# Optimization experiments

Hardware: AMD Instinct MI355X
Metric: run time of the kernel (lower is better)

The kernel has to match this reference:

```python
import jax, jax.numpy as jnp
import numpy as np

TEMPERATURE = 8.0  # sqrt(head_dim=64)

def setup_inputs() -> dict:
    key = jax.random.key(0)
    kq, kk, kv, km = jax.random.split(key, 4)
    B, H, S, D = 2, 16, 2048, 64
    q = jax.random.normal(kq, (B, H, S, D), dtype=jnp.float32)
    k = jax.random.normal(kk, (B, H, S, D), dtype=jnp.float32)
    v = jax.random.normal(kv, (B, H, S, D), dtype=jnp.float32)
    mask = jax.random.randint(km, (B, 1, 1, S), 0, 2, dtype=jnp.int32)
    return {"q": q, "k": k, "v": v, "mask": mask}

def reference(q, k, v, mask):
    # attn = softmax((q/T) @ k^T) with mask fill of -1e9 (dropout p=0 -> no-op)
    attn = jnp.einsum("bhsd,bhtd->bhst", q / TEMPERATURE, k)  # [B,H,S,S]
    attn = jnp.where(mask == 0, jnp.float32(-1e9), attn)
    attn = jax.nn.softmax(attn, axis=-1)
    # output = v^T @ attn @ v  -> [B,H,D,D]
    out = jnp.einsum("bhsd,bhst->bhdt", v, attn)   # v.transpose(2,3) @ attn
    out = jnp.einsum("bhdt,bhtc->bhdc", out, v)     # @ v
    return (out, attn)
```

## Files before the change

kernel.cpp:

```cpp
#include <hip/hip_runtime.h>
#include <math.h>

#define S_LEN 2048
#define D_DIM 64
#define NBH   32
#define TINV  0.125f

typedef float  f32x4  __attribute__((ext_vector_type(4)));
typedef short  s16x4  __attribute__((ext_vector_type(4)));
typedef short  s16x8  __attribute__((ext_vector_type(8)));
typedef __bf16 bf16x8 __attribute__((ext_vector_type(8)));

__device__ __forceinline__ short bfc(float f) {
  return __builtin_bit_cast(short, (__bf16)f);
}

__device__ __forceinline__ f32x4 mfma16(s16x8 a, s16x8 b, f32x4 c) {
  return __builtin_amdgcn_mfma_f32_16x16x32_bf16(
      __builtin_bit_cast(bf16x8, a), __builtin_bit_cast(bf16x8, b), c, 0, 0, 0);
}

__global__ __launch_bounds__(256) void prep(
    const float* __restrict__ k, const float* __restrict__ v,
    short* __restrict__ kb16, short* __restrict__ vT)
{
  const int bid = blockIdx.x;
  const int t   = bid & 1023;
  const int bh  = t >> 5;
  const int kt  = t & 31;
  const int tid = threadIdx.x;

  if (bid < 1024) {
    const int st  = tid >> 2;
    const int sd0 = (tid & 3) * 16;
    const float* kp = k + ((size_t)bh * S_LEN + kt * 64 + st) * D_DIM + sd0;
    s16x8 o0, o1;
    #pragma unroll
    for (int j = 0; j < 8; ++j) { o0[j] = bfc(kp[j]); o1[j] = bfc(kp[8 + j]); }
    short* dst = kb16 + ((size_t)bh * S_LEN + kt * 64 + st) * D_DIM + sd0;
    *(s16x8*)dst       = o0;
    *(s16x8*)(dst + 8) = o1;
  } else {
    const int vt0 = (tid & 15) * 4;
    const int vd0 = (tid >> 4) * 4;
    const float* vb = v + ((size_t)bh * S_LEN + kt * 64) * D_DIM;
    f32x4 vr[4];
    #pragma unroll
    for (int i = 0; i < 4; ++i)
      vr[i] = *(const f32x4*)(vb + (size_t)(vt0 + i) * D_DIM + vd0);
    #pragma unroll
    for (int j = 0; j < 4; ++j) {
      s16x4 pk;
      pk[0] = bfc(vr[0][j]); pk[1] = bfc(vr[1][j]);
      pk[2] = bfc(vr[2][j]); pk[3] = bfc(vr[3][j]);
      *(s16x4*)(vT + (size_t)(bh * 64 + vd0 + j) * S_LEN + kt * 64 + vt0) = pk;
    }
  }
}

__global__ __launch_bounds__(256, 4) void attn_fwd(
    const float* __restrict__ q, const short* __restrict__ kb16,
    const short* __restrict__ vT, const int* __restrict__ mask,
    float* __restrict__ attn_out, short* __restrict__ OT)
{
  __shared__ short Kl[64][72];
  __shared__ short Vl[64][72];
  __shared__ short Pl[4][16][72];

  const int bid   = blockIdx.x;
  const int xcd   = bid & 7;
  const int chunk = bid >> 3;
  const int bh    = xcd * 4 + (chunk >> 5);
  const int qt    = chunk & 31;
  const int b     = bh >> 4;

  const int tid  = threadIdx.x;
  const int wave = tid >> 6;
  const int lane = tid & 63;
  const int lr   = lane & 15;
  const int lg   = lane >> 4;
  const int wrow = qt * 64 + wave * 16;

  const short* kbb  = kb16 + (size_t)bh * S_LEN * D_DIM;
  const short* vtb  = vT   + (size_t)bh * 64 * S_LEN;
  const int*   mrow = mask + b * S_LEN;

  s16x8 aq[2];
  {
    const float* qp = q + ((size_t)bh * S_LEN + wrow + lr) * D_DIM + lg * 8;
    #pragma unroll
    for (int kk = 0; kk < 2; ++kk) {
      f32x4 a0 = *(const f32x4*)(qp + kk * 32);
      f32x4 a1 = *(const f32x4*)(qp + kk * 32 + 4);
      s16x8 f;
      #pragma unroll
      for (int j = 0; j < 4; ++j) { f[j] = bfc(a0[j]); f[4 + j] = bfc(a1[j]); }
      aq[kk] = f;
    }
  }

  f32x4 oacc[4];
  #pragma unroll
  for (int n = 0; n < 4; ++n) oacc[n] = (f32x4){0.f, 0.f, 0.f, 0.f};
  float rs = 0.f;

  const int st  = tid >> 2;
  const int sd0 = (tid & 3) * 16;

  s16x8 kr0, kr1, vr0, vr1;
  kr0 = *(const s16x8*)(kbb + (size_t)st * D_DIM + sd0);
  kr1 = *(const s16x8*)(kbb + (size_t)st * D_DIM + sd0 + 8);
  vr0 = *(const s16x8*)(vtb + (size_t)st * S_LEN + sd0);
  vr1 = *(const s16x8*)(vtb + (size_t)st * S_LEN + sd0 + 8);

  for (int kt = 0; kt < 32; ++kt) {
    __syncthreads();
    *(s16x8*)&Kl[st][sd0]     = kr0;
    *(s16x8*)&Kl[st][sd0 + 8] = kr1;
    *(s16x8*)&Vl[st][sd0]     = vr0;
    *(s16x8*)&Vl[st][sd0 + 8] = vr1;

    if (kt + 1 < 32) {
      kr0 = *(const s16x8*)(kbb + (size_t)((kt + 1) * 64 + st) * D_DIM + sd0);
      kr1 = *(const s16x8*)(kbb + (size_t)((kt + 1) * 64 + st) * D_DIM + sd0 + 8);
      vr0 = *(const s16x8*)(vtb + (size_t)st * S_LEN + (kt + 1) * 64 + sd0);
      vr1 = *(const s16x8*)(vtb + (size_t)st * S_LEN + (kt + 1) * 64 + sd0 + 8);
    }

    const unsigned long long mbits = __ballot(mrow[kt * 64 + lane] != 0);
    __syncthreads();

    #pragma unroll
    for (int n = 0; n < 4; ++n) {
      f32x4 sacc = (f32x4){0.f, 0.f, 0.f, 0.f};
      #pragma unroll
      for (int kk = 0; kk < 2; ++kk) {
        s16x8 bk = *(const s16x8*)&Kl[n * 16 + lr][kk * 32 + lg * 8];
        sacc = mfma16(bk, aq[kk], sacc);
      }
      const unsigned nib = (unsigned)(mbits >> (n * 16 + lg * 4)) & 0xFu;
      s16x4 pk;
      #pragma unroll
      for (int reg = 0; reg < 4; ++reg) {
        float e = __expf(sacc[reg] * TINV);
        float p = (nib & (1u << reg)) ? e : 0.f;
        rs += p;
        pk[reg] = bfc(p);
      }
      *(s16x4*)&Pl[wave][lr][n * 16 + lg * 4] = pk;
    }

    #pragma unroll
    for (int kk = 0; kk < 2; ++kk) {
      s16x8 ap = *(const s16x8*)&Pl[wave][lr][kk * 32 + lg * 8];
      #pragma unroll
      for (int n = 0; n < 4; ++n) {
        s16x8 bv = *(const s16x8*)&Vl[n * 16 + lr][kk * 32 + lg * 8];
        oacc[n] = mfma16(ap, bv, oacc[n]);
      }
    }
  }

  rs += __shfl_xor(rs, 16, 64);
  rs += __shfl_xor(rs, 32, 64);
  const float rinv = 1.0f / rs;

  float rinvO[4];
  #pragma unroll
  for (int reg = 0; reg < 4; ++reg)
    rinvO[reg] = __shfl(rinv, lg * 4 + reg, 64);

  #pragma unroll
  for (int n = 0; n < 4; ++n) {
    s16x4 ov;
    #pragma unroll
    for (int reg = 0; reg < 4; ++reg) ov[reg] = bfc(oacc[n][reg] * rinvO[reg]);
    short* dst = OT + (size_t)(bh * 64 + n * 16 + lr) * S_LEN + wrow + lg * 4;
    *(s16x4*)dst = ov;
  }

  float* ap_out = attn_out + (size_t)bh * S_LEN * S_LEN + (size_t)(wrow + lr) * S_LEN;

  for (int kt = 0; kt < 32; ++kt) {
    const unsigned long long mbits = __ballot(mrow[kt * 64 + lane] != 0);

    #pragma unroll
    for (int n = 0; n < 4; ++n) {
      f32x4 sacc = (f32x4){0.f, 0.f, 0.f, 0.f};
      #pragma unroll
      for (int kk = 0; kk < 2; ++kk) {
        s16x8 bk = *(const s16x8*)(kbb + (size_t)(kt * 64 + n * 16 + lr) * D_DIM +
                                   kk * 32 + lg * 8);
        sacc = mfma16(bk, aq[kk], sacc);
      }
      const unsigned nib = (unsigned)(mbits >> (n * 16 + lg * 4)) & 0xFu;
      f32x4 pv;
      #pragma unroll
      for (int reg = 0; reg < 4; ++reg) {
        float e = __expf(sacc[reg] * TINV);
        pv[reg] = (nib & (1u << reg)) ? e * rinv : 0.f;
      }
      __builtin_nontemporal_store(pv, (f32x4*)(ap_out + kt * 64 + n * 16 + lg * 4));
    }
  }
}

__global__ __launch_bounds__(256) void vo_gemm(
    const short* __restrict__ vT, const short* __restrict__ OT,
    float* __restrict__ out)
{
  const int bh   = blockIdx.x;
  const int tid  = threadIdx.x;
  const int wave = tid >> 6;
  const int lane = tid & 63;
  const int lr   = lane & 15;
  const int lg   = lane >> 4;

  const short* vb = vT + (size_t)(bh * 64) * S_LEN;
  const short* ob = OT + (size_t)(bh * 64) * S_LEN;

  f32x4 acc[4];
  #pragma unroll
  for (int n = 0; n < 4; ++n) acc[n] = (f32x4){0.f, 0.f, 0.f, 0.f};

  for (int s = 0; s < S_LEN; s += 32) {
    s16x8 a = *(const s16x8*)&vb[(size_t)(wave * 16 + lr) * S_LEN + s + lg * 8];
    #pragma unroll
    for (int n = 0; n < 4; ++n) {
      s16x8 bo = *(const s16x8*)&ob[(size_t)(n * 16 + lr) * S_LEN + s + lg * 8];
      acc[n] = mfma16(a, bo, acc[n]);
    }
  }

  #pragma unroll
  for (int n = 0; n < 4; ++n) {
    #pragma unroll
    for (int reg = 0; reg < 4; ++reg) {
      const int d = wave * 16 + lg * 4 + reg;
      const int c = n * 16 + lr;
      out[(size_t)(bh * 64 + d) * 64 + c] = acc[n][reg];
    }
  }
}

extern "C" void kernel_launch(void* const* d_in, const int* in_sizes, int n_in,
                              void* d_out, int out_size, void* d_ws, size_t ws_size,
                              hipStream_t stream) {
  (void)in_sizes; (void)n_in; (void)out_size; (void)ws_size;
  const float* q    = (const float*)d_in[0];
  const float* k    = (const float*)d_in[1];
  const float* v    = (const float*)d_in[2];
  const int*   mask = (const int*)d_in[3];

  float* out  = (float*)d_out;
  float* attn = out + (size_t)NBH * 64 * 64;

  short* OT   = (short*)d_ws;
  short* vT   = (short*)d_ws + (size_t)NBH * 64 * S_LEN;
  short* kb16 = (short*)d_ws + (size_t)NBH * 64 * S_LEN * 2;

  prep<<<dim3(2048), dim3(256), 0, stream>>>(k, v, kb16, vT);
  attn_fwd<<<dim3(1024), dim3(256), 0, stream>>>(q, kb16, vT, mask, attn, OT);
  vo_gemm<<<dim3(NBH), dim3(256), 0, stream>>>(vT, OT, out);
}
```

Baseline: 244.8 us.

## Use 32x32 MFMA with register P exchange and swizzled LDS in first pass

Rewrites the first attention pass to use 32x32x16 bf16 MFMAs. Waves are split into two query tiles by two key halves. The P tile is passed from the score MFMA to the PV MFMA through v_permlane32_swap instead of a per-wave LDS staging buffer, and K/V are stored in XOR-swizzled unpadded LDS to avoid bank conflicts. Partial row sums and output accumulators from the two key halves are reduced through LDS at the end. The aim is to raise MFMA efficiency and cut LDS traffic, at the cost of more registers, an extra cross-wave reduction and inline asm that only works on recent CDNA parts.

```diff
diff --git a/kernel.cpp b/kernel.cpp
--- a/kernel.cpp
+++ b/kernel.cpp
@@ -6,18 +6,31 @@
 #define NBH   32
 #define TINV  0.125f
 
-typedef float  f32x4  __attribute__((ext_vector_type(4)));
-typedef short  s16x4  __attribute__((ext_vector_type(4)));
-typedef short  s16x8  __attribute__((ext_vector_type(8)));
-typedef __bf16 bf16x8 __attribute__((ext_vector_type(8)));
+typedef float  f32x4   __attribute__((ext_vector_type(4)));
+typedef float  f32x16  __attribute__((ext_vector_type(16)));
+typedef short  s16x4   __attribute__((ext_vector_type(4)));
+typedef short  s16x8   __attribute__((ext_vector_type(8)));
+typedef unsigned u32x4 __attribute__((ext_vector_type(4)));
+typedef __bf16 bf16x8  __attribute__((ext_vector_type(8)));
 
 __device__ __forceinline__ short bfc(float f) {
   return __builtin_bit_cast(short, (__bf16)f);
+}
+__device__ __forceinline__ unsigned pk2(float lo, float hi) {
+  return (unsigned)(unsigned short)bfc(lo) | ((unsigned)(unsigned short)bfc(hi) << 16);
 }
 
 __device__ __forceinline__ f32x4 mfma16(s16x8 a, s16x8 b, f32x4 c) {
   return __builtin_amdgcn_mfma_f32_16x16x32_bf16(
       __builtin_bit_cast(bf16x8, a), __builtin_bit_cast(bf16x8, b), c, 0, 0, 0);
+}
+__device__ __forceinline__ f32x16 mfma32(s16x8 a, s16x8 b, f32x16 c) {
+  return __builtin_amdgcn_mfma_f32_32x32x16_bf16(
+      __builtin_bit_cast(bf16x8, a), __builtin_bit_cast(bf16x8, b), c, 0, 0, 0);
+}
+
+__device__ __forceinline__ short* ldsp(short* base, int row, int byteoff) {
+  return (short*)((char*)base + row * 128 + (byteoff ^ ((row & 7) << 4)));
 }
 
 __global__ __launch_bounds__(256) void prep(
@@ -63,9 +76,11 @@
     const short* __restrict__ vT, const int* __restrict__ mask,
     float* __restrict__ attn_out, short* __restrict__ OT)
 {
-  __shared__ short Kl[64][72];
-  __shared__ short Vl[64][72];
-  __shared__ short Pl[4][16][72];
+  __shared__ short KV[2][64][64];
+  __shared__ float rspart[4][32];
+
+  short* KlB = &KV[0][0][0];
+  short* VlB = &KV[1][0][0];
 
   const int bid   = blockIdx.x;
   const int xcd   = bid & 7;
@@ -79,107 +94,146 @@
   const int lane = tid & 63;
   const int lr   = lane & 15;
   const int lg   = lane >> 4;
-  const int wrow = qt * 64 + wave * 16;
+  const int L31  = lane & 31;
+  const int hi   = lane >> 5;
+  const int Q0   = qt * 64;
+
+  const int qtile = wave & 1;
+  const int tt    = wave >> 1;
 
   const short* kbb  = kb16 + (size_t)bh * S_LEN * D_DIM;
   const short* vtb  = vT   + (size_t)bh * 64 * S_LEN;
   const int*   mrow = mask + b * S_LEN;
 
+  s16x8 aqv[4];
+  {
+    const float* qp = q + ((size_t)bh * S_LEN + Q0 + qtile * 32 + L31) * D_DIM + hi * 8;
+    #pragma unroll
+    for (int ks = 0; ks < 4; ++ks) {
+      f32x4 x0 = *(const f32x4*)(qp + ks * 16);
+      f32x4 x1 = *(const f32x4*)(qp + ks * 16 + 4);
+      s16x8 f;
+      #pragma unroll
+      for (int j = 0; j < 4; ++j) { f[j] = bfc(x0[j]); f[4 + j] = bfc(x1[j]); }
+      aqv[ks] = f;
+    }
+  }
+
+  f32x16 oacc[2];
+  #pragma unroll
+  for (int dt = 0; dt < 2; ++dt)
+    #pragma unroll
+    for (int r = 0; r < 16; ++r) oacc[dt][r] = 0.f;
+  float rs = 0.f;
+
+  const int st = tid >> 2;
+  const int c0 = (tid & 3) * 32;
+
+  s16x8 kr0, kr1, vr0, vr1;
+  kr0 = *(const s16x8*)(kbb + (size_t)st * D_DIM + c0 / 2);
+  kr1 = *(const s16x8*)(kbb + (size_t)st * D_DIM + c0 / 2 + 8);
+  vr0 = *(const s16x8*)(vtb + (size_t)st * S_LEN + c0 / 2);
+  vr1 = *(const s16x8*)(vtb + (size_t)st * S_LEN + c0 / 2 + 8);
+
+  for (int kt = 0; kt < 32; ++kt) {
+    __syncthreads();
+    *(s16x8*)ldsp(KlB, st, c0)      = kr0;
+    *(s16x8*)ldsp(KlB, st, c0 + 16) = kr1;
+    *(s16x8*)ldsp(VlB, st, c0)      = vr0;
+    *(s16x8*)ldsp(VlB, st, c0 + 16) = vr1;
+    __syncthreads();
+
+    if (kt + 1 < 32) {
+      kr0 = *(const s16x8*)(kbb + (size_t)((kt + 1) * 64 + st) * D_DIM + c0 / 2);
+      kr1 = *(const s16x8*)(kbb + (size_t)((kt + 1) * 64 + st) * D_DIM + c0 / 2 + 8);
+      vr0 = *(const s16x8*)(vtb + (size_t)st * S_LEN + (kt + 1) * 64 + c0 / 2);
+      vr1 = *(const s16x8*)(vtb + (size_t)st * S_LEN + (kt + 1) * 64 + c0 / 2 + 8);
+    }
+    const unsigned long long mbits = __ballot(mrow[kt * 64 + lane] != 0);
+
+    f32x16 sacc;
+    #pragma unroll
+    for (int r = 0; r < 16; ++r) sacc[r] = 0.f;
+    #pragma unroll
+    for (int ks = 0; ks < 4; ++ks) {
+      s16x8 ak = *(const s16x8*)ldsp(KlB, tt * 32 + L31, ks * 32 + hi * 16);
+      sacc = mfma32(ak, aqv[ks], sacc);
+    }
+
+    const unsigned mloc = (unsigned)(mbits >> (tt * 32 + hi * 4));
+    #pragma unroll
+    for (int r = 0; r < 16; ++r) {
+      float e = __expf(sacc[r] * TINV);
+      e = ((mloc >> ((r & 3) + 8 * (r >> 2))) & 1u) ? e : 0.f;
+      rs += e;
+      sacc[r] = e;
+    }
+
+    unsigned a0 = pk2(sacc[0], sacc[1]),   b0 = pk2(sacc[4], sacc[5]);
+    unsigned a1 = pk2(sacc[2], sacc[3]),   b1 = pk2(sacc[6], sacc[7]);
+    unsigned a2 = pk2(sacc[8], sacc[9]),   b2 = pk2(sacc[12], sacc[13]);
+    unsigned a3 = pk2(sacc[10], sacc[11]), b3 = pk2(sacc[14], sacc[15]);
+    asm volatile("v_permlane32_swap_b32 %0, %1" : "+v"(a0), "+v"(b0));
+    asm volatile("v_permlane32_swap_b32 %0, %1" : "+v"(a1), "+v"(b1));
+    asm volatile("v_permlane32_swap_b32 %0, %1" : "+v"(a2), "+v"(b2));
+    asm volatile("v_permlane32_swap_b32 %0, %1" : "+v"(a3), "+v"(b3));
+    const s16x8 pb0 = __builtin_bit_cast(s16x8, (u32x4){a0, a1, b0, b1});
+    const s16x8 pb1 = __builtin_bit_cast(s16x8, (u32x4){a2, a3, b2, b3});
+
+    #pragma unroll
+    for (int dt = 0; dt < 2; ++dt) {
+      s16x8 bv0 = *(const s16x8*)ldsp(VlB, dt * 32 + L31, tt * 64 + hi * 16);
+      s16x8 bv1 = *(const s16x8*)ldsp(VlB, dt * 32 + L31, tt * 64 + 32 + hi * 16);
+      oacc[dt] = mfma32(bv0, pb0, oacc[dt]);
+      oacc[dt] = mfma32(bv1, pb1, oacc[dt]);
+    }
+  }
+
+  rs += __shfl_xor(rs, 32, 64);
+
+  __syncthreads();
+  if (lane < 32) rspart[wave][lane] = rs;
+  float* oex = (float*)&KV[0][0][0];
+  if (wave >= 2) {
+    #pragma unroll
+    for (int dt = 0; dt < 2; ++dt)
+      #pragma unroll
+      for (int r = 0; r < 16; ++r)
+        oex[(wave - 2) * 2048 + dt * 1024 + r * 64 + lane] = oacc[dt][r];
+  }
+  __syncthreads();
+
+  if (wave < 2) {
+    const float rinvq = 1.0f / (rspart[wave][L31] + rspart[wave + 2][L31]);
+    #pragma unroll
+    for (int dt = 0; dt < 2; ++dt)
+      #pragma unroll
+      for (int r = 0; r < 16; ++r) {
+        const int d = dt * 32 + (r & 3) + 8 * (r >> 2) + 4 * hi;
+        float val = (oacc[dt][r] + oex[wave * 2048 + dt * 1024 + r * 64 + lane]) * rinvq;
+        OT[(size_t)(bh * 64 + d) * S_LEN + Q0 + wave * 32 + L31] = bfc(val);
+      }
+  }
+
+  const int qin = (wave & 1) * 16 + lr;
+  const float rinv = 1.0f / (rspart[wave >> 1][qin] + rspart[(wave >> 1) + 2][qin]);
+
   s16x8 aq[2];
   {
-    const float* qp = q + ((size_t)bh * S_LEN + wrow + lr) * D_DIM + lg * 8;
+    const float* qp = q + ((size_t)bh * S_LEN + Q0 + wave * 16 + lr) * D_DIM + lg * 8;
     #pragma unroll
     for (int kk = 0; kk < 2; ++kk) {
-      f32x4 a0 = *(const f32x4*)(qp + kk * 32);
-      f32x4 a1 = *(const f32x4*)(qp + kk * 32 + 4);
+      f32x4 x0 = *(const f32x4*)(qp + kk * 32);
+      f32x4 x1 = *(const f32x4*)(qp + kk * 32 + 4);
       s16x8 f;
       #pragma unroll
-      for (int j = 0; j < 4; ++j) { f[j] = bfc(a0[j]); f[4 + j] = bfc(a1[j]); }
+      for (int j = 0; j < 4; ++j) { f[j] = bfc(x0[j]); f[4 + j] = bfc(x1[j]); }
       aq[kk] = f;
     }
   }
 
-  f32x4 oacc[4];
-  #pragma unroll
-  for (int n = 0; n < 4; ++n) oacc[n] = (f32x4){0.f, 0.f, 0.f, 0.f};
-  float rs = 0.f;
-
-  const int st  = tid >> 2;
-  const int sd0 = (tid & 3) * 16;
-
-  s16x8 kr0, kr1, vr0, vr1;
-  kr0 = *(const s16x8*)(kbb + (size_t)st * D_DIM + sd0);
-  kr1 = *(const s16x8*)(kbb + (size_t)st * D_DIM + sd0 + 8);
-  vr0 = *(const s16x8*)(vtb + (size_t)st * S_LEN + sd0);
-  vr1 = *(const s16x8*)(vtb + (size_t)st * S_LEN + sd0 + 8);
-
-  for (int kt = 0; kt < 32; ++kt) {
-    __syncthreads();
-    *(s16x8*)&Kl[st][sd0]     = kr0;
-    *(s16x8*)&Kl[st][sd0 + 8] = kr1;
-    *(s16x8*)&Vl[st][sd0]     = vr0;
-    *(s16x8*)&Vl[st][sd0 + 8] = vr1;
-
-    if (kt + 1 < 32) {
-      kr0 = *(const s16x8*)(kbb + (size_t)((kt + 1) * 64 + st) * D_DIM + sd0);
-      kr1 = *(const s16x8*)(kbb + (size_t)((kt + 1) * 64 + st) * D_DIM + sd0 + 8);
-      vr0 = *(const s16x8*)(vtb + (size_t)st * S_LEN + (kt + 1) * 64 + sd0);
-      vr1 = *(const s16x8*)(vtb + (size_t)st * S_LEN + (kt + 1) * 64 + sd0 + 8);
-    }
-
-    const unsigned long long mbits = __ballot(mrow[kt * 64 + lane] != 0);
-    __syncthreads();
-
-    #pragma unroll
-    for (int n = 0; n < 4; ++n) {
-      f32x4 sacc = (f32x4){0.f, 0.f, 0.f, 0.f};
-      #pragma unroll
-      for (int kk = 0; kk < 2; ++kk) {
-        s16x8 bk = *(const s16x8*)&Kl[n * 16 + lr][kk * 32 + lg * 8];
-        sacc = mfma16(bk, aq[kk], sacc);
-      }
-      const unsigned nib = (unsigned)(mbits >> (n * 16 + lg * 4)) & 0xFu;
-      s16x4 pk;
-      #pragma unroll
-      for (int reg = 0; reg < 4; ++reg) {
-        float e = __expf(sacc[reg] * TINV);
-        float p = (nib & (1u << reg)) ? e : 0.f;
-        rs += p;
-        pk[reg] = bfc(p);
-      }
-      *(s16x4*)&Pl[wave][lr][n * 16 + lg * 4] = pk;
-    }
-
-    #pragma unroll
-    for (int kk = 0; kk < 2; ++kk) {
-      s16x8 ap = *(const s16x8*)&Pl[wave][lr][kk * 32 + lg * 8];
-      #pragma unroll
-      for (int n = 0; n < 4; ++n) {
-        s16x8 bv = *(const s16x8*)&Vl[n * 16 + lr][kk * 32 + lg * 8];
-        oacc[n] = mfma16(ap, bv, oacc[n]);
-      }
-    }
-  }
-
-  rs += __shfl_xor(rs, 16, 64);
-  rs += __shfl_xor(rs, 32, 64);
-  const float rinv = 1.0f / rs;
-
-  float rinvO[4];
-  #pragma unroll
-  for (int reg = 0; reg < 4; ++reg)
-    rinvO[reg] = __shfl(rinv, lg * 4 + reg, 64);
-
-  #pragma unroll
-  for (int n = 0; n < 4; ++n) {
-    s16x4 ov;
-    #pragma unroll
-    for (int reg = 0; reg < 4; ++reg) ov[reg] = bfc(oacc[n][reg] * rinvO[reg]);
-    short* dst = OT + (size_t)(bh * 64 + n * 16 + lr) * S_LEN + wrow + lg * 4;
-    *(s16x4*)dst = ov;
-  }
-
-  float* ap_out = attn_out + (size_t)bh * S_LEN * S_LEN + (size_t)(wrow + lr) * S_LEN;
+  float* ap_out = attn_out + (size_t)bh * S_LEN * S_LEN +
+                  (size_t)(Q0 + wave * 16 + lr) * S_LEN;
 
   for (int kt = 0; kt < 32; ++kt) {
     const unsigned long long mbits = __ballot(mrow[kt * 64 + lane] != 0);
```

After: 241.3 us. No clear change (-1.4%).
